# Kernel optimization log

Measured on AMD Instinct MI355X. Metric: run time of the kernel, lower is better.

The kernel has to match this reference:

```python
import jax, jax.numpy as jnp
import numpy as np

VOCAB = 100000
E = 256      # embedding dim == projection dim (required by layer-axis concat)
H = 2048     # lstm hidden dim
P = 256      # projection dim
B, T = 8, 96
CELL_CLIP = 3.0
PROJ_CLIP = 3.0
NUM_LAYERS = 2


def setup_inputs() -> dict:
    key = jax.random.key(0)
    ks = jax.random.split(key, 8)
    tokens = jax.random.randint(ks[0], (B, T), 0, VOCAB, dtype=jnp.int32)
    mask = jnp.ones((B, T, 1), dtype=jnp.float32)
    embed_table = jax.random.normal(ks[1], (VOCAB + 1, E), dtype=jnp.float32) * 0.05
    # stacked LSTM weights: index 0=fwd L0, 1=fwd L1, 2=bwd L0, 3=bwd L1
    Wk = jax.random.normal(ks[2], (4, E, 4 * H), dtype=jnp.float32) * 0.02
    Wr = jax.random.normal(ks[3], (4, P, 4 * H), dtype=jnp.float32) * 0.02
    b = jnp.zeros((4, 4 * H), dtype=jnp.float32)
    Wp = jax.random.normal(ks[4], (4, H, P), dtype=jnp.float32) * 0.02
    elmo_w = jnp.zeros((NUM_LAYERS + 1,), dtype=jnp.float32)
    gamma = jnp.ones((1,), dtype=jnp.float32)
    return {"tokens": tokens, "mask": mask, "embed_table": embed_table,
            "Wk": Wk, "Wr": Wr, "b": b, "Wp": Wp,
            "elmo_w": elmo_w, "gamma": gamma}


def _lstm_proj(x, m, Wk, Wr, b, Wp, reverse):
    # x: [B,T,E], m: [B,T,1]. LSTM with cell clip, output projection, proj clip.
    if reverse:
        x = jnp.flip(x, 1)
        m = jnp.flip(m, 1)
    xs = jnp.swapaxes(x, 0, 1)                     # [T,B,E]
    ms = jnp.swapaxes(m, 0, 1)                     # [T,B,1]
    xW = jnp.einsum('tbe,ef->tbf', xs, Wk) + b     # precompute input gates [T,B,4H]

    def step(carry, inp):
        h, c = carry                               # h:[B,P], c:[B,H]
        zx, mt = inp
        z = zx + h @ Wr                            # [B,4H]
        i, f, g, o = jnp.split(z, 4, axis=-1)
        i = jax.nn.sigmoid(i)
        f = jax.nn.sigmoid(f)
        g = jnp.tanh(g)
        o = jax.nn.sigmoid(o)
        c_new = jnp.clip(f * c + i * g, -CELL_CLIP, CELL_CLIP)
        h_new = jnp.clip((o * jnp.tanh(c_new)) @ Wp, -PROJ_CLIP, PROJ_CLIP)
        keep = mt > 0
        h_new = jnp.where(keep, h_new, h)
        c_new = jnp.where(keep, c_new, c)
        return (h_new, c_new), h_new

    h0 = jnp.zeros((x.shape[0], Wp.shape[1]), x.dtype)
    c0 = jnp.zeros((x.shape[0], Wp.shape[0]), x.dtype)
    _, hs = jax.lax.scan(step, (h0, c0), (xW, ms))
    out = jnp.swapaxes(hs, 0, 1)                   # [B,T,P]
    if reverse:
        out = jnp.flip(out, 1)
    return out


def _elmo_layers(tokens, mask, embed_table, Wk, Wr, b, Wp):
    emb = embed_table[tokens]                      # [B,T,E]
    dir_outs = []
    for rev, base in ((False, 0), (True, 2)):
        inp = emb
        outs = []
        for l in range(NUM_LAYERS):
            out = _lstm_proj(inp, mask, Wk[base + l], Wr[base + l],
                             b[base + l], Wp[base + l], rev)
            inp = inp + out if l > 0 else out      # skip connection on layer > 0
            outs.append(inp)
        dir_outs.append(outs)
    fwd, bwd = dir_outs
    layers = [jnp.concatenate([emb, emb], -1)]
    layers += [jnp.concatenate([f, bb], -1) for f, bb in zip(fwd, bwd)]
    return jnp.stack(layers, axis=1)               # [B, L+1, T, 2P]


def reference(tokens, mask, embed_table, Wk, Wr, b, Wp, elmo_w, gamma):
    all_emb = _elmo_layers(tokens, mask, embed_table, Wk, Wr, b, Wp)
    m = mask[:, None, :, :]                        # [B,1,T,1]
    num = jnp.sum(mask, axis=(1, 2))[:, None]      # [B,1]
    xm = all_emb * m
    mean = jnp.sum(xm, axis=(2, 3)) / num          # [B,L+1]
    mean = mean[:, :, None, None]
    var = jnp.sum(((xm - mean) * m) ** 2, axis=(2, 3)) / num
    var = var[:, :, None, None]
    normed = (all_emb - mean) / jnp.sqrt(var + 1e-12)
    w = jax.nn.softmax(elmo_w)[None, :, None, None]
    weighted = jnp.sum(w * normed, axis=1) * gamma  # [B,T,2P]
    return weighted
```

## Files before the change

### kernel.cpp

```cpp
#include <hip/hip_runtime.h>
#include <hip/hip_bf16.h>

#define DEVFN __device__ __forceinline__

static constexpr size_t OFF_CTRS   = 0;
static constexpr size_t OFF_FLAG   = 131072;
static constexpr size_t OFF_STATS  = 131328;
static constexpr size_t OFF_EW     = 131584;
static constexpr size_t OFF_MASK32 = 131840;
static constexpr size_t OFF_EMB    = 135168;
static constexpr size_t OFF_WPT    = 921600;
static constexpr size_t OFF_BIAS   = 9310208;
static constexpr size_t OFF_XW     = 9441280;
static constexpr size_t OFF_OUT0   = 59772928;
static constexpr size_t OFF_OUT1   = 61345792;
static constexpr size_t OFF_Y      = 62918656;
static constexpr size_t OFF_H      = 75501568;

template<int BF>
DEVFN float ldin(const void* p, size_t i) {
  if (BF) {
    unsigned short u = ((const unsigned short*)p)[i];
    return __uint_as_float(((unsigned)u) << 16);
  }
  return ((const float*)p)[i];
}
DEVFN float ldraw(const void* p, size_t i, int bf) {
  if (bf) {
    unsigned short u = ((const unsigned short*)p)[i];
    return __uint_as_float(((unsigned)u) << 16);
  }
  return ((const float*)p)[i];
}

DEVFN float sigm(float x) { return 1.f / (1.f + __expf(-x)); }
DEVFN float clip3(float x) { return fminf(fmaxf(x, -3.f), 3.f); }

__global__ void detect_k(const unsigned* mask_raw, int* flagp) {
  if (threadIdx.x == 0) *flagp = (mask_raw[0] == 0x3F800000u) ? 0 : 1;
}

template<int BF>
__global__ void convert_k(const int* flagp, const void* bias, const void* mask,
                          const void* ew, const void* gm,
                          float* bias32, float* mask32, float* ew32) {
  if (*flagp != BF) return;
  size_t i = (size_t)blockIdx.x * 256 + threadIdx.x;
  if (i >= 33540) return;
  if (i < 32768)       bias32[i] = ldin<BF>(bias, i);
  else if (i < 33536)  mask32[i - 32768] = ldin<BF>(mask, i - 32768);
  else if (i < 33539)  ew32[i - 33536]   = ldin<BF>(ew, i - 33536);
  else                 ew32[3] = ldin<BF>(gm, 0);
}

template<int BF>
__global__ void transpose_wp_k(const int* flagp, const void* Wp, float* WpT) {
  if (*flagp != BF) return;
  const int kt = blockIdx.x, pt = blockIdx.y, dl = blockIdx.z;
  __shared__ float tile[64][65];
  const int tid = threadIdx.x;
  for (int it = 0; it < 4; ++it) {
    int lin = it * 1024 + tid * 4;
    int kk = lin >> 6, pp = lin & 63;
    size_t src = ((size_t)(dl * 2048 + kt * 64 + kk)) * 256 + pt * 64 + pp;
    float v0, v1, v2, v3;
    if (BF) {
      const unsigned short* sp = (const unsigned short*)Wp + src;
      v0 = __uint_as_float(((unsigned)sp[0]) << 16);
      v1 = __uint_as_float(((unsigned)sp[1]) << 16);
      v2 = __uint_as_float(((unsigned)sp[2]) << 16);
      v3 = __uint_as_float(((unsigned)sp[3]) << 16);
    } else {
      float4 v = *(const float4*)((const float*)Wp + src);
      v0 = v.x; v1 = v.y; v2 = v.z; v3 = v.w;
    }
    tile[pp + 0][kk] = v0; tile[pp + 1][kk] = v1; tile[pp + 2][kk] = v2; tile[pp + 3][kk] = v3;
  }
  __syncthreads();
  for (int it = 0; it < 4; ++it) {
    int lin = it * 1024 + tid * 4;
    int pr = lin >> 6, kc = lin & 63;
    float4 o;
    o.x = tile[pr][kc + 0]; o.y = tile[pr][kc + 1]; o.z = tile[pr][kc + 2]; o.w = tile[pr][kc + 3];
    *(float4*)(WpT + ((size_t)(dl * 256 + pt * 64 + pr)) * 2048 + kt * 64 + kc) = o;
  }
}

template<int BF>
__global__ void gather_k(const int* flagp, const int* tokens, const void* et, float* emb) {
  if (*flagp != BF) return;
  const int bt = blockIdx.x;
  const int tok = tokens[bt];
  emb[(size_t)bt * 256 + threadIdx.x] = ldin<BF>(et, (size_t)tok * 256 + threadIdx.x);
}

template<int BF>
__global__ __launch_bounds__(256) void xw_gemm_k(
    const int* __restrict__ flagp, const float* __restrict__ x_fwd, const float* __restrict__ x_bwd,
    const void* __restrict__ Wk, const float* __restrict__ bias32, float* __restrict__ xW, int layer) {
  if (*flagp != BF) return;
  const int nt = blockIdx.x, mt = blockIdx.y, dir = blockIdx.z;
  const int dl = dir * 2 + layer;
  const float* xb = dir ? x_bwd : x_fwd;
  const int tid = threadIdx.x;

  __shared__ float As[16][68];
  __shared__ float Bs[16][68];

  float acc[4][4] = {};
  const int tx = tid & 15, ty = tid >> 4;

  const int am = tid >> 2;
  const int ak = (tid & 3) * 4;
  const int m_glob = mt * 64 + am;
  const int t_ = m_glob >> 3, b_ = m_glob & 7;
  const int tau = dir ? (95 - t_) : t_;
  const float* arow = xb + ((size_t)(b_ * 96 + tau)) * 256;

  const int bk = tid >> 4, bn = (tid & 15) * 4;

  for (int kb = 0; kb < 256; kb += 16) {
    float4 av = *(const float4*)(arow + kb + ak);
    As[ak + 0][am] = av.x; As[ak + 1][am] = av.y; As[ak + 2][am] = av.z; As[ak + 3][am] = av.w;

    size_t bidx = ((size_t)dl * 256 + (kb + bk)) * 8192 + (size_t)nt * 64 + bn;
    float b0, b1, b2, b3;
    if (BF) {
      ushort4 uv = *(const ushort4*)((const unsigned short*)Wk + bidx);
      b0 = __uint_as_float(((unsigned)uv.x) << 16);
      b1 = __uint_as_float(((unsigned)uv.y) << 16);
      b2 = __uint_as_float(((unsigned)uv.z) << 16);
      b3 = __uint_as_float(((unsigned)uv.w) << 16);
    } else {
      float4 fv = *(const float4*)((const float*)Wk + bidx);
      b0 = fv.x; b1 = fv.y; b2 = fv.z; b3 = fv.w;
    }
    Bs[bk][bn + 0] = b0; Bs[bk][bn + 1] = b1; Bs[bk][bn + 2] = b2; Bs[bk][bn + 3] = b3;
    __syncthreads();

#pragma unroll
    for (int kk = 0; kk < 16; ++kk) {
      float a0 = As[kk][ty * 4 + 0], a1 = As[kk][ty * 4 + 1], a2 = As[kk][ty * 4 + 2], a3 = As[kk][ty * 4 + 3];
      float c0 = Bs[kk][tx * 4 + 0], c1 = Bs[kk][tx * 4 + 1], c2 = Bs[kk][tx * 4 + 2], c3 = Bs[kk][tx * 4 + 3];
      acc[0][0] = fmaf(a0, c0, acc[0][0]); acc[0][1] = fmaf(a0, c1, acc[0][1]);
      acc[0][2] = fmaf(a0, c2, acc[0][2]); acc[0][3] = fmaf(a0, c3, acc[0][3]);
      acc[1][0] = fmaf(a1, c0, acc[1][0]); acc[1][1] = fmaf(a1, c1, acc[1][1]);
      acc[1][2] = fmaf(a1, c2, acc[1][2]); acc[1][3] = fmaf(a1, c3, acc[1][3]);
      acc[2][0] = fmaf(a2, c0, acc[2][0]); acc[2][1] = fmaf(a2, c1, acc[2][1]);
      acc[2][2] = fmaf(a2, c2, acc[2][2]); acc[2][3] = fmaf(a2, c3, acc[2][3]);
      acc[3][0] = fmaf(a3, c0, acc[3][0]); acc[3][1] = fmaf(a3, c1, acc[3][1]);
      acc[3][2] = fmaf(a3, c2, acc[3][2]); acc[3][3] = fmaf(a3, c3, acc[3][3]);
    }
    __syncthreads();
  }

  const int n0 = nt * 64 + tx * 4;
#pragma unroll
  for (int i = 0; i < 4; ++i) {
    int m = mt * 64 + ty * 4 + i;
    int tt = m >> 3, bb = m & 7;
    float4 o;
    o.x = acc[i][0] + bias32[dl * 8192 + n0 + 0];
    o.y = acc[i][1] + bias32[dl * 8192 + n0 + 1];
    o.z = acc[i][2] + bias32[dl * 8192 + n0 + 2];
    o.w = acc[i][3] + bias32[dl * 8192 + n0 + 3];
    *(float4*)(xW + (size_t)((dir * 96 + tt) * 8 + bb) * 8192 + n0) = o;
  }
}

DEVFN void wg_barrier(int* base, int g, int bcnt) {
  __syncthreads();
  if (threadIdx.x == 0) {
    const int grp = g >> 3;
    int* gctr  = base + grp * 64;
    int* root  = base + 32 * 64;
    int* gflag = base + (33 + grp) * 64;
    int old = __hip_atomic_fetch_add(gctr, 1, __ATOMIC_RELAXED, __HIP_MEMORY_SCOPE_AGENT);
    if (old == 8 * bcnt - 1)
      __hip_atomic_fetch_add(root, 1, __ATOMIC_RELAXED, __HIP_MEMORY_SCOPE_AGENT);
    if ((g & 7) == 0) {
      while (__hip_atomic_load(root, __ATOMIC_RELAXED, __HIP_MEMORY_SCOPE_AGENT) < 32 * bcnt)
        __builtin_amdgcn_s_sleep(1);
      __hip_atomic_store(gflag, bcnt, __ATOMIC_RELAXED, __HIP_MEMORY_SCOPE_AGENT);
    } else {
      while (__hip_atomic_load(gflag, __ATOMIC_RELAXED, __HIP_MEMORY_SCOPE_AGENT) < bcnt)
        __builtin_amdgcn_s_sleep(1);
    }
  }
  __syncthreads();
}

__global__ __launch_bounds__(256, 2) void scan_kernel(
    const float* __restrict__ xW, const void* __restrict__ WrRaw, const int* __restrict__ flagp,
    const float* __restrict__ WpT, const float* __restrict__ mask32,
    float* __restrict__ out, float* __restrict__ hbuf, float* __restrict__ ybuf,
    int* ctrs, int layer) {
  const int tid = threadIdx.x;
  const int w = blockIdx.x;
  const int dir = w >> 8;
  const int g = w & 255;
  const int dl = dir * 2 + layer;

  __shared__ float  wr_s[256 * 36];
  __shared__ float  h_lds[2048];
  __shared__ float4 zred[256];
  __shared__ float  z_s[8][4][8];
  __shared__ float  c_s[64];
  __shared__ float4 wp_sp[576];
  __shared__ float  red[256];

  int* base = ctrs + (layer * 2 + dir) * 65 * 64;
  int bcnt = 0;

  const int bf = *flagp;
  {
    const size_t wrbase = (size_t)dl * 256 * 8192;
    for (int i = tid; i < 8192; i += 256) {
      int k = i >> 5, c = i & 31;
      size_t gidx = wrbase + (size_t)k * 8192 + (size_t)(c >> 3) * 2048 + g * 8 + (c & 7);
      wr_s[k * 36 + c] = ldraw(WrRaw, gidx, bf);
    }
  }
  {
    const float4* wrow = (const float4*)(WpT + ((size_t)(dl * 256 + g)) * 2048);
    for (int i = tid; i < 512; i += 256)
      wp_sp[i + (i >> 3)] = wrow[i];
  }
  if (tid < 64) c_s[tid] = 0.f;

  const int u = tid >> 2, ks = tid & 3;
  const int ub = u >> 3, ugate = (u >> 1) & 3, uq = u & 1;
  const int c0 = ugate * 8 + uq * 4;

  for (int t = 0; t < 96; ++t) {
    const int tau = dir ? (95 - t) : t;
    const float* h_cur = hbuf + ((size_t)(t * 2 + dir)) * 2048;
    float* h_nxt = hbuf + ((size_t)((t + 1) * 2 + dir)) * 2048;
    float* y_t   = ybuf + ((size_t)(t * 2 + dir)) * 16384;

    for (int i = tid; i < 2048; i += 256) h_lds[i] = (t == 0) ? 0.f : h_cur[i];
    __syncthreads();

    {
      float4 acc = make_float4(0.f, 0.f, 0.f, 0.f);
      const float* hrow = h_lds + ub * 256;
#pragma unroll 8
      for (int i = 0; i < 64; ++i) {
        int k = (i << 2) + ks;
        float hv = hrow[k];
        float4 wv = *(const float4*)&wr_s[k * 36 + c0];
        acc.x = fmaf(hv, wv.x, acc.x); acc.y = fmaf(hv, wv.y, acc.y);
        acc.z = fmaf(hv, wv.z, acc.z); acc.w = fmaf(hv, wv.w, acc.w);
      }
      zred[tid] = acc;
    }
    __syncthreads();

    if (tid < 64) {
      float4 s0 = zred[tid * 4 + 0], s1 = zred[tid * 4 + 1], s2 = zred[tid * 4 + 2], s3 = zred[tid * 4 + 3];
      float sx = s0.x + s1.x + s2.x + s3.x;
      float sy = s0.y + s1.y + s2.y + s3.y;
      float sz = s0.z + s1.z + s2.z + s3.z;
      float sw = s0.w + s1.w + s2.w + s3.w;
      const int b2 = tid >> 3, gate2 = (tid >> 1) & 3, q2 = tid & 1;
      const int colq2 = gate2 * 512 + g * 2 + q2;
      float4 xv = ((const float4*)xW)[(size_t)((dir * 96 + t) * 8 + b2) * 2048 + colq2];
      z_s[b2][gate2][q2 * 4 + 0] = sx + xv.x;
      z_s[b2][gate2][q2 * 4 + 1] = sy + xv.y;
      z_s[b2][gate2][q2 * 4 + 2] = sz + xv.z;
      z_s[b2][gate2][q2 * 4 + 3] = sw + xv.w;
    }
    __syncthreads();

    if (tid < 64) {
      const int b3 = tid >> 3, cell = tid & 7;
      float zi = z_s[b3][0][cell], zf = z_s[b3][1][cell], zg = z_s[b3][2][cell], zo = z_s[b3][3][cell];
      float ig = sigm(zi), fg = sigm(zf), gg = tanhf(zg), og = sigm(zo);
      float cold = c_s[tid];
      float cc = clip3(fg * cold + ig * gg);
      float yv = og * tanhf(cc);
      float m = mask32[b3 * 96 + tau];
      c_s[tid] = (m > 0.f) ? cc : cold;
      __hip_atomic_store(&y_t[b3 * 2048 + g * 8 + cell], yv, __ATOMIC_RELAXED, __HIP_MEMORY_SCOPE_AGENT);
    }
    wg_barrier(base, g, ++bcnt);

    {
      const int b = tid >> 5, kk = tid & 31;
      const float4* yb = (const float4*)(y_t + b * 2048);
      float f = 0.f;
#pragma unroll 4
      for (int i = 0; i < 16; ++i) {
        int k4 = kk + (i << 5);
        float4 yv = yb[k4];
        float4 wv = wp_sp[k4 + (k4 >> 3)];
        f = fmaf(yv.x, wv.x, f); f = fmaf(yv.y, wv.y, f);
        f = fmaf(yv.z, wv.z, f); f = fmaf(yv.w, wv.w, f);
      }
      red[kk * 8 + b] = f;
    }
    __syncthreads();
    if (tid < 8) {
      float s = 0.f;
#pragma unroll 8
      for (int i = 0; i < 32; ++i) s += red[i * 8 + tid];
      float hc = clip3(s);
      float m = mask32[tid * 96 + tau];
      float hp = (t == 0) ? 0.f : h_cur[tid * 256 + g];
      float hv = (m > 0.f) ? hc : hp;
      __hip_atomic_store(&h_nxt[tid * 256 + g], hv, __ATOMIC_RELAXED, __HIP_MEMORY_SCOPE_AGENT);
      out[(size_t)((dir * 8 + tid) * 96 + tau) * 256 + g] = hv;
    }
    wg_barrier(base, g, ++bcnt);
  }
}

DEVFN float layer_val(int l, int b, int t, int f, const float* emb, const float* out0, const float* out1) {
  const int half = f >> 8, p = f & 255;
  if (l == 0) return emb[(size_t)(b * 96 + t) * 256 + p];
  const size_t o = ((size_t)((half * 8 + b) * 96 + t)) * 256 + p;
  float v = out0[o];
  if (l == 2) v += out1[o];
  return v;
}

__global__ void mixA_k(const float* emb, const float* out0, const float* out1,
                       const float* mask32, float* stats) {
  const int b = blockIdx.x / 3, l = blockIdx.x % 3;
  float s1 = 0.f, s2 = 0.f;
  for (int idx = threadIdx.x; idx < 96 * 512; idx += 256) {
    int t = idx >> 9, f = idx & 511;
    float v = layer_val(l, b, t, f, emb, out0, out1);
    float m = mask32[b * 96 + t];
    s1 += m * v; s2 += m * v * v;
  }
  for (int off = 32; off; off >>= 1) { s1 += __shfl_down(s1, off); s2 += __shfl_down(s2, off); }
  __shared__ float p1[4], p2[4];
  if ((threadIdx.x & 63) == 0) { p1[threadIdx.x >> 6] = s1; p2[threadIdx.x >> 6] = s2; }
  __syncthreads();
  if (threadIdx.x == 0) {
    float S1 = p1[0] + p1[1] + p1[2] + p1[3];
    float S2 = p2[0] + p2[1] + p2[2] + p2[3];
    float num = 0.f;
    for (int t = 0; t < 96; ++t) num += mask32[b * 96 + t];
    float mean = S1 / num;
    float var = S2 / num - 2.f * mean * mean + 512.f * mean * mean;
    stats[(b * 3 + l) * 2 + 0] = mean;
    stats[(b * 3 + l) * 2 + 1] = rsqrtf(var + 1e-12f);
  }
}

__global__ void mixB_k(const int* flagp, const float* emb, const float* out0, const float* out1,
                       const float* stats, const float* ew32, void* outp) {
  const int idx = blockIdx.x * 256 + threadIdx.x;
  const int b = idx / 49152;
  const int r = idx % 49152;
  const int t = r >> 9, f = r & 511;
  float w0 = ew32[0], w1 = ew32[1], w2 = ew32[2], gm = ew32[3];
  float mx = fmaxf(w0, fmaxf(w1, w2));
  float e0 = __expf(w0 - mx), e1 = __expf(w1 - mx), e2 = __expf(w2 - mx);
  float inv = 1.f / (e0 + e1 + e2);
  float wl[3] = {e0 * inv, e1 * inv, e2 * inv};
  float acc = 0.f;
#pragma unroll
  for (int l = 0; l < 3; ++l) {
    float v = layer_val(l, b, t, f, emb, out0, out1);
    acc += wl[l] * (v - stats[(b * 3 + l) * 2]) * stats[(b * 3 + l) * 2 + 1];
  }
  acc *= gm;
  if (*flagp) ((__hip_bfloat16*)outp)[idx] = __float2bfloat16(acc);
  else        ((float*)outp)[idx] = acc;
}

extern "C" void kernel_launch(void* const* d_in, const int* in_sizes, int n_in,
                              void* d_out, int out_size, void* d_ws, size_t ws_size,
                              hipStream_t stream) {
  const int*  tokens = (const int*)d_in[0];
  const void* maskp  = d_in[1];
  const void* embt   = d_in[2];
  const void* Wk     = d_in[3];
  const void* WrRaw  = d_in[4];
  const void* bias   = d_in[5];
  const void* Wp     = d_in[6];
  const void* ew     = d_in[7];
  const void* gm     = d_in[8];

  char* ws = (char*)d_ws;
  int*   ctrs   = (int*)(ws + OFF_CTRS);
  int*   flagp  = (int*)(ws + OFF_FLAG);
  float* stats  = (float*)(ws + OFF_STATS);
  float* ew32   = (float*)(ws + OFF_EW);
  float* mask32 = (float*)(ws + OFF_MASK32);
  float* emb    = (float*)(ws + OFF_EMB);
  float* wpt    = (float*)(ws + OFF_WPT);
  float* bias32 = (float*)(ws + OFF_BIAS);
  float* xW     = (float*)(ws + OFF_XW);
  float* out0   = (float*)(ws + OFF_OUT0);
  float* out1   = (float*)(ws + OFF_OUT1);
  float* ybuf   = (float*)(ws + OFF_Y);
  float* hbuf   = (float*)(ws + OFF_H);

  hipMemsetAsync(d_ws, 0, 131072, stream);
  detect_k<<<1, 64, 0, stream>>>((const unsigned*)maskp, flagp);

  convert_k<0><<<132, 256, 0, stream>>>(flagp, bias, maskp, ew, gm, bias32, mask32, ew32);
  convert_k<1><<<132, 256, 0, stream>>>(flagp, bias, maskp, ew, gm, bias32, mask32, ew32);

  transpose_wp_k<0><<<dim3(32, 4, 4), 256, 0, stream>>>(flagp, Wp, wpt);
  transpose_wp_k<1><<<dim3(32, 4, 4), 256, 0, stream>>>(flagp, Wp, wpt);

  gather_k<0><<<768, 256, 0, stream>>>(flagp, tokens, embt, emb);
  gather_k<1><<<768, 256, 0, stream>>>(flagp, tokens, embt, emb);

  xw_gemm_k<0><<<dim3(128, 12, 2), 256, 0, stream>>>(flagp, emb, emb, Wk, bias32, xW, 0);
  xw_gemm_k<1><<<dim3(128, 12, 2), 256, 0, stream>>>(flagp, emb, emb, Wk, bias32, xW, 0);

  int l0 = 0, l1 = 1;
  {
    void* args[] = {&xW, &WrRaw, &flagp, &wpt, &mask32, &out0, &hbuf, &ybuf, &ctrs, &l0};
    hipError_t e = hipLaunchCooperativeKernel((void*)scan_kernel, dim3(512), dim3(256), args, 0, stream);
    if (e != hipSuccess)
      scan_kernel<<<512, 256, 0, stream>>>(xW, WrRaw, flagp, wpt, mask32, out0, hbuf, ybuf, ctrs, 0);
  }

  float* x_fwd = out0;
  float* x_bwd = out0 + (size_t)8 * 96 * 256;
  xw_gemm_k<0><<<dim3(128, 12, 2), 256, 0, stream>>>(flagp, x_fwd, x_bwd, Wk, bias32, xW, 1);
  xw_gemm_k<1><<<dim3(128, 12, 2), 256, 0, stream>>>(flagp, x_fwd, x_bwd, Wk, bias32, xW, 1);

  {
    void* args[] = {&xW, &WrRaw, &flagp, &wpt, &mask32, &out1, &hbuf, &ybuf, &ctrs, &l1};
    hipError_t e = hipLaunchCooperativeKernel((void*)scan_kernel, dim3(512), dim3(256), args, 0, stream);
    if (e != hipSuccess)
      scan_kernel<<<512, 256, 0, stream>>>(xW, WrRaw, flagp, wpt, mask32, out1, hbuf, ybuf, ctrs, 1);
  }

  mixA_k<<<24, 256, 0, stream>>>(emb, out0, out1, mask32, stats);
  mixB_k<<<1536, 256, 0, stream>>>(flagp, emb, out0, out1, stats, ew32, d_out);
}
```

Before: 2.863 ms.

## Flatten grid barrier, transpose h layout, prefetch xW and reduce with shuffles

The hierarchical two-level grid barrier becomes a flat one: every block's leader now spins directly on the root counter instead of waiting for a group flag. That removes one propagation hop per barrier but puts more pollers on a single atomic. The recurrent state h is stored batch-innermost (index g*8+b), and the recurrent matvec is remapped so each thread covers a k-range for one batch and column quad. The per-step xW slice is loaded early into LDS, and mask is cached in LDS. The projection reduction uses warp shuffles instead of an LDS reduction, and one synchronisation point is dropped by merging the gate-sum and cell-update phases.

New measurement: 2.997 ms. 1.05x slower.

```diff
diff --git a/kernel.cpp b/kernel.cpp
--- a/kernel.cpp
+++ b/kernel.cpp
@@ -171,21 +171,13 @@
 DEVFN void wg_barrier(int* base, int g, int bcnt) {
   __syncthreads();
   if (threadIdx.x == 0) {
-    const int grp = g >> 3;
-    int* gctr  = base + grp * 64;
-    int* root  = base + 32 * 64;
-    int* gflag = base + (33 + grp) * 64;
+    int* gctr = base + (g >> 3) * 64;
+    int* root = base + 32 * 64;
     int old = __hip_atomic_fetch_add(gctr, 1, __ATOMIC_RELAXED, __HIP_MEMORY_SCOPE_AGENT);
     if (old == 8 * bcnt - 1)
       __hip_atomic_fetch_add(root, 1, __ATOMIC_RELAXED, __HIP_MEMORY_SCOPE_AGENT);
-    if ((g & 7) == 0) {
-      while (__hip_atomic_load(root, __ATOMIC_RELAXED, __HIP_MEMORY_SCOPE_AGENT) < 32 * bcnt)
-        __builtin_amdgcn_s_sleep(1);
-      __hip_atomic_store(gflag, bcnt, __ATOMIC_RELAXED, __HIP_MEMORY_SCOPE_AGENT);
-    } else {
-      while (__hip_atomic_load(gflag, __ATOMIC_RELAXED, __HIP_MEMORY_SCOPE_AGENT) < bcnt)
-        __builtin_amdgcn_s_sleep(1);
-    }
+    while (__hip_atomic_load(root, __ATOMIC_RELAXED, __HIP_MEMORY_SCOPE_AGENT) < 32 * bcnt)
+      __builtin_amdgcn_s_sleep(1);
   }
   __syncthreads();
 }
@@ -201,36 +193,35 @@
   const int g = w & 255;
   const int dl = dir * 2 + layer;
 
-  __shared__ float  wr_s[256 * 36];
-  __shared__ float  h_lds[2048];
-  __shared__ float4 zred[256];
-  __shared__ float  z_s[8][4][8];
+  __shared__ __align__(16) float wr_s[256 * 32];
+  __shared__ __align__(16) float h_lds[2048];
+  __shared__ float4 wp4_s[512];
+  __shared__ float4 zpart[288];
+  __shared__ float  z_s[32 * 9];
+  __shared__ __align__(16) float xw_s[256];
+  __shared__ float  mask_s[768];
   __shared__ float  c_s[64];
-  __shared__ float4 wp_sp[576];
-  __shared__ float  red[256];
+  __shared__ float  red_s[8];
 
   int* base = ctrs + (layer * 2 + dir) * 65 * 64;
   int bcnt = 0;
-
   const int bf = *flagp;
+
   {
     const size_t wrbase = (size_t)dl * 256 * 8192;
     for (int i = tid; i < 8192; i += 256) {
-      int k = i >> 5, c = i & 31;
-      size_t gidx = wrbase + (size_t)k * 8192 + (size_t)(c >> 3) * 2048 + g * 8 + (c & 7);
-      wr_s[k * 36 + c] = ldraw(WrRaw, gidx, bf);
-    }
-  }
-  {
+      int k = i >> 5, col = i & 31;
+      wr_s[i] = ldraw(WrRaw, wrbase + (size_t)k * 8192 + (size_t)(col >> 3) * 2048 + g * 8 + (col & 7), bf);
+    }
     const float4* wrow = (const float4*)(WpT + ((size_t)(dl * 256 + g)) * 2048);
-    for (int i = tid; i < 512; i += 256)
-      wp_sp[i + (i >> 3)] = wrow[i];
+    for (int i = tid; i < 512; i += 256) wp4_s[i] = wrow[i];
+    for (int i = tid; i < 768; i += 256) mask_s[i] = mask32[i];
   }
   if (tid < 64) c_s[tid] = 0.f;
 
-  const int u = tid >> 2, ks = tid & 3;
-  const int ub = u >> 3, ugate = (u >> 1) & 3, uq = u & 1;
-  const int c0 = ugate * 8 + uq * 4;
+  const int ks = tid >> 6, colq = (tid >> 3) & 7, lb = tid & 7;
+  const float4* wr4 = (const float4*)wr_s;
+  const float4* xw4 = (const float4*)xw_s;
 
   for (int t = 0; t < 96; ++t) {
     const int tau = dir ? (95 - t) : t;
@@ -238,77 +229,88 @@
     float* h_nxt = hbuf + ((size_t)((t + 1) * 2 + dir)) * 2048;
     float* y_t   = ybuf + ((size_t)(t * 2 + dir)) * 16384;
 
-    for (int i = tid; i < 2048; i += 256) h_lds[i] = (t == 0) ? 0.f : h_cur[i];
+    float xwv;
+    {
+      int b = tid >> 5, col = tid & 31;
+      xwv = xW[(size_t)((dir * 96 + t) * 8 + b) * 8192 + (col >> 3) * 2048 + g * 8 + (col & 7)];
+    }
+
+    if (t == 0) {
+      ((float4*)h_lds)[tid * 2 + 0] = make_float4(0.f, 0.f, 0.f, 0.f);
+      ((float4*)h_lds)[tid * 2 + 1] = make_float4(0.f, 0.f, 0.f, 0.f);
+    } else {
+      ((float4*)h_lds)[tid * 2 + 0] = ((const float4*)h_cur)[tid * 2 + 0];
+      ((float4*)h_lds)[tid * 2 + 1] = ((const float4*)h_cur)[tid * 2 + 1];
+    }
     __syncthreads();
 
     {
       float4 acc = make_float4(0.f, 0.f, 0.f, 0.f);
-      const float* hrow = h_lds + ub * 256;
-#pragma unroll 8
+#pragma unroll 16
       for (int i = 0; i < 64; ++i) {
-        int k = (i << 2) + ks;
-        float hv = hrow[k];
-        float4 wv = *(const float4*)&wr_s[k * 36 + c0];
+        int k = (ks << 6) + i;
+        float hv = h_lds[k * 8 + lb];
+        float4 wv = wr4[k * 8 + colq];
         acc.x = fmaf(hv, wv.x, acc.x); acc.y = fmaf(hv, wv.y, acc.y);
         acc.z = fmaf(hv, wv.z, acc.z); acc.w = fmaf(hv, wv.w, acc.w);
       }
-      zred[tid] = acc;
+      zpart[(ks * 8 + colq) * 9 + lb] = acc;
+      xw_s[tid] = xwv;
     }
     __syncthreads();
 
     if (tid < 64) {
-      float4 s0 = zred[tid * 4 + 0], s1 = zred[tid * 4 + 1], s2 = zred[tid * 4 + 2], s3 = zred[tid * 4 + 3];
-      float sx = s0.x + s1.x + s2.x + s3.x;
-      float sy = s0.y + s1.y + s2.y + s3.y;
-      float sz = s0.z + s1.z + s2.z + s3.z;
-      float sw = s0.w + s1.w + s2.w + s3.w;
-      const int b2 = tid >> 3, gate2 = (tid >> 1) & 3, q2 = tid & 1;
-      const int colq2 = gate2 * 512 + g * 2 + q2;
-      float4 xv = ((const float4*)xW)[(size_t)((dir * 96 + t) * 8 + b2) * 2048 + colq2];
-      z_s[b2][gate2][q2 * 4 + 0] = sx + xv.x;
-      z_s[b2][gate2][q2 * 4 + 1] = sy + xv.y;
-      z_s[b2][gate2][q2 * 4 + 2] = sz + xv.z;
-      z_s[b2][gate2][q2 * 4 + 3] = sw + xv.w;
-    }
-    __syncthreads();
-
-    if (tid < 64) {
-      const int b3 = tid >> 3, cell = tid & 7;
-      float zi = z_s[b3][0][cell], zf = z_s[b3][1][cell], zg = z_s[b3][2][cell], zo = z_s[b3][3][cell];
+      const int b3 = tid & 7, cq = tid >> 3;
+      float4 z0 = zpart[(0 * 8 + cq) * 9 + b3];
+      float4 z1 = zpart[(1 * 8 + cq) * 9 + b3];
+      float4 z2 = zpart[(2 * 8 + cq) * 9 + b3];
+      float4 z3 = zpart[(3 * 8 + cq) * 9 + b3];
+      float4 xv = xw4[b3 * 8 + cq];
+      z_s[(cq * 4 + 0) * 9 + b3] = z0.x + z1.x + z2.x + z3.x + xv.x;
+      z_s[(cq * 4 + 1) * 9 + b3] = z0.y + z1.y + z2.y + z3.y + xv.y;
+      z_s[(cq * 4 + 2) * 9 + b3] = z0.z + z1.z + z2.z + z3.z + xv.z;
+      z_s[(cq * 4 + 3) * 9 + b3] = z0.w + z1.w + z2.w + z3.w + xv.w;
+      const int cell = cq;
+      float zi = z_s[(0  + cell) * 9 + b3];
+      float zf = z_s[(8  + cell) * 9 + b3];
+      float zg = z_s[(16 + cell) * 9 + b3];
+      float zo = z_s[(24 + cell) * 9 + b3];
       float ig = sigm(zi), fg = sigm(zf), gg = tanhf(zg), og = sigm(zo);
       float cold = c_s[tid];
       float cc = clip3(fg * cold + ig * gg);
       float yv = og * tanhf(cc);
-      float m = mask32[b3 * 96 + tau];
+      float m = mask_s[b3 * 96 + tau];
       c_s[tid] = (m > 0.f) ? cc : cold;
       __hip_atomic_store(&y_t[b3 * 2048 + g * 8 + cell], yv, __ATOMIC_RELAXED, __HIP_MEMORY_SCOPE_AGENT);
     }
     wg_barrier(base, g, ++bcnt);
 
     {
-      const int b = tid >> 5, kk = tid & 31;
-      const float4* yb = (const float4*)(y_t + b * 2048);
-      float f = 0.f;
+      const int b = tid >> 5, kq = tid & 31;
+      const float4* yb = (const float4*)y_t + b * 512;
+      float s = 0.f;
 #pragma unroll 4
       for (int i = 0; i < 16; ++i) {
-        int k4 = kk + (i << 5);
+        int k4 = i * 32 + kq;
         float4 yv = yb[k4];
-        float4 wv = wp_sp[k4 + (k4 >> 3)];
-        f = fmaf(yv.x, wv.x, f); f = fmaf(yv.y, wv.y, f);
-        f = fmaf(yv.z, wv.z, f); f = fmaf(yv.w, wv.w, f);
+        float4 wv = wp4_s[k4];
+        s = fmaf(yv.x, wv.x, s); s = fmaf(yv.y, wv.y, s);
+        s = fmaf(yv.z, wv.z, s); s = fmaf(yv.w, wv.w, s);
       }
-      red[kk * 8 + b] = f;
+      s += __shfl_down(s, 16, 32);
+      s += __shfl_down(s, 8, 32);
+      s += __shfl_down(s, 4, 32);
+      s += __shfl_down(s, 2, 32);
+      s += __shfl_down(s, 1, 32);
+      if (kq == 0) red_s[b] = s;
     }
     __syncthreads();
     if (tid < 8) {
-      float s = 0.f;
-#pragma unroll 8
-      for (int i = 0; i < 32; ++i) s += red[i * 8 + tid];
-      float hc = clip3(s);
-      float m = mask32[tid * 96 + tau];
-      float hp = (t == 0) ? 0.f : h_cur[tid * 256 + g];
+      float hc = clip3(red_s[tid]);
+      float m = mask_s[tid * 96 + tau];
+      float hp = h_lds[g * 8 + tid];
       float hv = (m > 0.f) ? hc : hp;
-      __hip_atomic_store(&h_nxt[tid * 256 + g], hv, __ATOMIC_RELAXED, __HIP_MEMORY_SCOPE_AGENT);
+      __hip_atomic_store(&h_nxt[g * 8 + tid], hv, __ATOMIC_RELAXED, __HIP_MEMORY_SCOPE_AGENT);
       out[(size_t)((dir * 8 + tid) * 96 + tau) * 256 + g] = hv;
     }
     wg_barrier(base, g, ++bcnt);
```
